# Performance work log

Measured on AMD Instinct MI355X. Metric: run time of the kernel, lower is better.

The kernel has to match this reference:

```python
import jax, jax.numpy as jnp
import numpy as np

B, T, C, H = 2, 2048, 1024, 16
HD = C // H  # head size = 64
EPS = 1e-5


def setup_inputs() -> dict:
    key = jax.random.key(0)
    ks = jax.random.split(key, 16)
    s = 0.02
    return {
        "x": jax.random.normal(ks[0], (B, T, C), jnp.float32),
        # per-head q/k/v projections, stacked: [H, C, HD]
        "Wq": jax.random.normal(ks[1], (H, C, HD), jnp.float32) * s,
        "Wk": jax.random.normal(ks[2], (H, C, HD), jnp.float32) * s,
        "Wv": jax.random.normal(ks[3], (H, C, HD), jnp.float32) * s,
        "Wproj": jax.random.normal(ks[4], (C, C), jnp.float32) * s,
        "bproj": jnp.zeros((C,), jnp.float32),
        "W1": jax.random.normal(ks[5], (C, 4 * C), jnp.float32) * s,
        "b1": jnp.zeros((4 * C,), jnp.float32),
        "W2": jax.random.normal(ks[6], (4 * C, C), jnp.float32) * s,
        "b2": jnp.zeros((C,), jnp.float32),
        "g1": jnp.ones((C,), jnp.float32),
        "be1": jnp.zeros((C,), jnp.float32),
        "g2": jnp.ones((C,), jnp.float32),
        "be2": jnp.zeros((C,), jnp.float32),
    }


def _layernorm(x, g, b):
    mu = jnp.mean(x, axis=-1, keepdims=True)
    var = jnp.mean(jnp.square(x - mu), axis=-1, keepdims=True)
    return (x - mu) * jax.lax.rsqrt(var + EPS) * g + b


def _block(x, Wq, Wk, Wv, Wproj, bproj, W1, b1, W2, b2, g1, be1, g2, be2):
    Bx, Tx, Cx = x.shape
    h = _layernorm(x, g1, be1)
    q = jnp.einsum("btc,hcd->bhtd", h, Wq)
    k = jnp.einsum("btc,hcd->bhtd", h, Wk)
    v = jnp.einsum("btc,hcd->bhtd", h, Wv)
    scores = jnp.einsum("bhtd,bhsd->bhts", q, k) * (HD ** -0.5)  # [B,H,T,T]
    causal = jnp.tril(jnp.ones((Tx, Tx), bool))
    scores = jnp.where(causal, scores, -jnp.inf)
    w = jax.nn.softmax(scores, axis=-1)
    o = jnp.einsum("bhts,bhsd->bhtd", w, v)
    o = o.transpose(0, 2, 1, 3).reshape(Bx, Tx, Cx)  # concat heads
    x = x + o @ Wproj + bproj
    h2 = _layernorm(x, g2, be2)
    ff = jax.nn.relu(h2 @ W1 + b1) @ W2 + b2
    return x + ff


def reference(x, Wq, Wk, Wv, Wproj, bproj, W1, b1, W2, b2, g1, be1, g2, be2):
    return _block(x, Wq, Wk, Wv, Wproj, bproj, W1, b1, W2, b2, g1, be1, g2, be2)
```

## Files before the change

### kernel.cpp

```cpp
#include <hip/hip_runtime.h>
#include <stdint.h>


typedef unsigned short u16;
typedef unsigned int u32;
typedef __attribute__((ext_vector_type(4))) float f32x4;
typedef __attribute__((ext_vector_type(8))) short s16x8;

__device__ __forceinline__ u16 f2bf(float f) {
  u32 u = __builtin_bit_cast(u32, f);
  u += 0x7fffu + ((u >> 16) & 1u);
  return (u16)(u >> 16);
}
__device__ __forceinline__ s16x8 ld_s16x8_a8(const u16* p) {
  union { uint2 d[2]; s16x8 v; } u;
  u.d[0] = *(const uint2*)p;
  u.d[1] = *(const uint2*)(p + 4);
  return u.v;
}
__device__ __forceinline__ void gload16(const u16* g, u16* lds_base) {
  __builtin_amdgcn_global_load_lds(
      (const __attribute__((address_space(1))) void*)g,
      (__attribute__((address_space(3))) void*)lds_base, 16, 0, 0);
}

__global__ __launch_bounds__(256) void transpose_all_kernel(
    const float* __restrict__ Wq, const float* __restrict__ Wk,
    const float* __restrict__ Wv, const float* __restrict__ Wproj,
    const float* __restrict__ W1, const float* __restrict__ W2,
    u16* __restrict__ WqkvT, u16* __restrict__ WprojT,
    u16* __restrict__ W1T, u16* __restrict__ W2T) {
  const int bid = blockIdx.x;
  const float* src; u16* dst; int Ccols, dstStride, r0, c0;
  if (bid < 768) {
    const int sub = bid >> 8, rem = bid & 255;
    const int z = rem >> 4, y = rem & 15;
    src = (sub == 0 ? Wq : sub == 1 ? Wk : Wv) + (size_t)z * 65536;
    dst = WqkvT + (size_t)sub * 1024 * 1024 + (size_t)z * 65536;
    Ccols = 64; dstStride = 1024; r0 = y * 64; c0 = 0;
  } else if (bid < 1024) {
    const int rem = bid - 768, xx = rem & 15, y = rem >> 4;
    src = Wproj; dst = WprojT; Ccols = 1024; dstStride = 1024;
    r0 = y * 64; c0 = xx * 64;
  } else if (bid < 2048) {
    const int rem = bid - 1024, xx = rem & 63, y = rem >> 6;
    src = W1; dst = W1T; Ccols = 4096; dstStride = 1024;
    r0 = y * 64; c0 = xx * 64;
  } else {
    const int rem = bid - 2048, xx = rem & 15, y = rem >> 4;
    src = W2; dst = W2T; Ccols = 1024; dstStride = 4096;
    r0 = y * 64; c0 = xx * 64;
  }
  __shared__ float t[64][65];
  const int tr = threadIdx.x >> 4, tc4 = (threadIdx.x & 15) * 4;
#pragma unroll
  for (int p = 0; p < 4; ++p) {
    int r = p * 16 + tr;
    float4 v = *(const float4*)(src + (size_t)(r0 + r) * Ccols + c0 + tc4);
    t[r][tc4 + 0] = v.x; t[r][tc4 + 1] = v.y;
    t[r][tc4 + 2] = v.z; t[r][tc4 + 3] = v.w;
  }
  __syncthreads();
#pragma unroll
  for (int p = 0; p < 4; ++p) {
    int c = p * 16 + tr;
    uint2 pk;
    pk.x = (u32)f2bf(t[tc4 + 0][c]) | ((u32)f2bf(t[tc4 + 1][c]) << 16);
    pk.y = (u32)f2bf(t[tc4 + 2][c]) | ((u32)f2bf(t[tc4 + 3][c]) << 16);
    *(uint2*)(dst + (size_t)(c0 + c) * dstStride + r0 + tc4) = pk;
  }
}

__global__ __launch_bounds__(256) void ln_kernel(
    const float* __restrict__ x, const float* __restrict__ g,
    const float* __restrict__ be, u16* __restrict__ out) {
  const int row = blockIdx.x, tid = threadIdx.x;
  const float* xr = x + (size_t)row * 1024;
  float4 v = *(const float4*)(xr + tid * 4);
  float s = v.x + v.y + v.z + v.w;
  float q = v.x * v.x + v.y * v.y + v.z * v.z + v.w * v.w;
#pragma unroll
  for (int off = 32; off > 0; off >>= 1) {
    s += __shfl_down(s, off);
    q += __shfl_down(q, off);
  }
  __shared__ float red[8];
  const int wid = tid >> 6, lane = tid & 63;
  if (lane == 0) { red[wid] = s; red[wid + 4] = q; }
  __syncthreads();
  s = red[0] + red[1] + red[2] + red[3];
  q = red[4] + red[5] + red[6] + red[7];
  const float mu = s * (1.f / 1024.f);
  const float var = q * (1.f / 1024.f) - mu * mu;
  const float rs = rsqrtf(var + 1e-5f);
  float4 gv = *(const float4*)(g + tid * 4);
  float4 bv = *(const float4*)(be + tid * 4);
  float o0 = (v.x - mu) * rs * gv.x + bv.x;
  float o1 = (v.y - mu) * rs * gv.y + bv.y;
  float o2 = (v.z - mu) * rs * gv.z + bv.z;
  float o3 = (v.w - mu) * rs * gv.w + bv.w;
  uint2 pk;
  pk.x = (u32)f2bf(o0) | ((u32)f2bf(o1) << 16);
  pk.y = (u32)f2bf(o2) | ((u32)f2bf(o3) << 16);
  *(uint2*)(out + (size_t)row * 1024 + tid * 4) = pk;
}

__global__ __launch_bounds__(256) void combine_kernel(
    const float* __restrict__ P, const float* __restrict__ resid,
    const float* __restrict__ bias, float* __restrict__ out) {
  const int row = blockIdx.x, c4 = threadIdx.x * 4;
  const size_t idx = (size_t)row * 1024 + c4;
  float4 p0 = *(const float4*)(P + idx);
  float4 p1 = *(const float4*)(P + 4194304 + idx);
  float4 r  = *(const float4*)(resid + idx);
  float4 bb = *(const float4*)(bias + c4);
  float4 o;
  o.x = p0.x + p1.x + r.x + bb.x;
  o.y = p0.y + p1.y + r.y + bb.y;
  o.z = p0.z + p1.z + r.z + bb.z;
  o.w = p0.w + p1.w + r.w + bb.w;
  *(float4*)(out + idx) = o;
}

template <int EPI>
__global__ __launch_bounds__(512, 2) void gemm256_kernel(
    const u16* __restrict__ A, const u16* __restrict__ BT,
    const float* __restrict__ bias, const float* __restrict__ resid,
    void* __restrict__ out, int M, int N, int K) {
  __shared__ u16 lds[2][2][256][64];
  const int tid = threadIdx.x;
  const int wid = tid >> 6, lane = tid & 63;
  const int m0 = blockIdx.y * 256, n0 = blockIdx.x * 256;
  const int wr = (wid >> 2) * 128;
  const int wc = (wid & 3) * 64;
  const int l15 = lane & 15, g = lane >> 4;
  const int lr = lane >> 3;
  const int cswz = ((lane & 7) * 8) ^ (lr << 3);
  const int swz = (l15 & 7) << 3;
  const u16* Abase = A + (size_t)m0 * K;
  const u16* Bbase = BT + (size_t)n0 * K;
  const int nkt = K >> 6;

  f32x4 acc[8][4] = {};
  s16x8 bf[4][2];

  auto issue_half = [&](const u16* Xbase, int xi, int t, int hf) {
    const int b = t & 1;
    const int r0 = hf * 128 + wid * 8;
    gload16(Xbase + (size_t)(r0 + lr) * K + t * 64 + cswz, &lds[b][xi][r0][0]);
    gload16(Xbase + (size_t)(r0 + 64 + lr) * K + t * 64 + cswz, &lds[b][xi][r0 + 64][0]);
  };

  issue_half(Abase, 0, 0, 0);
  issue_half(Abase, 0, 0, 1);
  issue_half(Bbase, 1, 0, 0);
  issue_half(Bbase, 1, 0, 1);
  asm volatile("s_waitcnt vmcnt(0)" ::: "memory");
  __builtin_amdgcn_s_barrier();

  for (int i = 0; i < nkt; i += 2) {
#pragma unroll
    for (int p = 0; p < 4; ++p) {
      s16x8 af[2][2];
#pragma unroll
      for (int q = 0; q < 2; ++q) {
        const int R = wr + (2 * p + q) * 16 + l15;
#pragma unroll
        for (int h = 0; h < 2; ++h)
          af[q][h] = *(const s16x8*)(&lds[0][0][R][(h * 32 + g * 8) ^ swz]);
      }
      if (p == 0) {
#pragma unroll
        for (int n = 0; n < 4; ++n) {
          const int R = wc + n * 16 + l15;
#pragma unroll
          for (int h = 0; h < 2; ++h)
            bf[n][h] = *(const s16x8*)(&lds[0][1][R][(h * 32 + g * 8) ^ swz]);
        }
      }
      if (i + 1 < nkt) {
        if (p == 0) issue_half(Abase, 0, i + 1, 0);
        else if (p == 1) issue_half(Abase, 0, i + 1, 1);
        else if (p == 2) issue_half(Bbase, 1, i + 1, 0);
        else issue_half(Bbase, 1, i + 1, 1);
      }
      __builtin_amdgcn_s_barrier();
      asm volatile("s_waitcnt lgkmcnt(0)" ::: "memory");
      __builtin_amdgcn_sched_barrier(0);
      __builtin_amdgcn_s_setprio(1);
#pragma unroll
      for (int q = 0; q < 2; ++q)
#pragma unroll
        for (int n = 0; n < 4; ++n) {
          acc[2 * p + q][n] = __builtin_amdgcn_mfma_f32_16x16x32_bf16(af[q][0], bf[n][0], acc[2 * p + q][n], 0, 0, 0);
          acc[2 * p + q][n] = __builtin_amdgcn_mfma_f32_16x16x32_bf16(af[q][1], bf[n][1], acc[2 * p + q][n], 0, 0, 0);
        }
      __builtin_amdgcn_s_setprio(0);
      if (p == 3)
        asm volatile("s_waitcnt vmcnt(0)" ::: "memory");
      __builtin_amdgcn_s_barrier();
    }
    if (i + 1 < nkt) {
#pragma unroll
      for (int p = 0; p < 4; ++p) {
        s16x8 af[2][2];
#pragma unroll
        for (int q = 0; q < 2; ++q) {
          const int R = wr + (2 * p + q) * 16 + l15;
#pragma unroll
          for (int h = 0; h < 2; ++h)
            af[q][h] = *(const s16x8*)(&lds[1][0][R][(h * 32 + g * 8) ^ swz]);
        }
        if (p == 0) {
#pragma unroll
          for (int n = 0; n < 4; ++n) {
            const int R = wc + n * 16 + l15;
#pragma unroll
            for (int h = 0; h < 2; ++h)
              bf[n][h] = *(const s16x8*)(&lds[1][1][R][(h * 32 + g * 8) ^ swz]);
          }
        }
        if (i + 2 < nkt) {
          if (p == 0) issue_half(Abase, 0, i + 2, 0);
          else if (p == 1) issue_half(Abase, 0, i + 2, 1);
          else if (p == 2) issue_half(Bbase, 1, i + 2, 0);
          else issue_half(Bbase, 1, i + 2, 1);
        }
        __builtin_amdgcn_s_barrier();
        asm volatile("s_waitcnt lgkmcnt(0)" ::: "memory");
        __builtin_amdgcn_sched_barrier(0);
        __builtin_amdgcn_s_setprio(1);
#pragma unroll
        for (int q = 0; q < 2; ++q)
#pragma unroll
          for (int n = 0; n < 4; ++n) {
            acc[2 * p + q][n] = __builtin_amdgcn_mfma_f32_16x16x32_bf16(af[q][0], bf[n][0], acc[2 * p + q][n], 0, 0, 0);
            acc[2 * p + q][n] = __builtin_amdgcn_mfma_f32_16x16x32_bf16(af[q][1], bf[n][1], acc[2 * p + q][n], 0, 0, 0);
          }
        __builtin_amdgcn_s_setprio(0);
        if (p == 3)
          asm volatile("s_waitcnt vmcnt(0)" ::: "memory");
        __builtin_amdgcn_s_barrier();
      }
    }
  }

#pragma unroll
  for (int mi = 0; mi < 8; ++mi)
#pragma unroll
    for (int n = 0; n < 4; ++n) {
      const int col = n0 + wc + n * 16 + l15;
      float bv = (EPI >= 1) ? bias[col] : 0.f;
#pragma unroll
      for (int ii = 0; ii < 4; ++ii) {
        const int row = m0 + wr + mi * 16 + g * 4 + ii;
        float v = acc[mi][n][ii];
        if (EPI >= 1) v += bv;
        if (EPI == 1) v = fmaxf(v, 0.f);
        ((u16*)out)[(size_t)row * N + col] = f2bf(v);
      }
    }
}

template <int EPI>
__global__ __launch_bounds__(256, 2) void gemm128d_kernel(
    const u16* __restrict__ A, const u16* __restrict__ BT,
    const float* __restrict__ bias, const float* __restrict__ resid,
    void* __restrict__ out, int M, int N, int K, int lda) {
  __shared__ u16 lds[2][2][128][64];
  const int tid = threadIdx.x;
  const int wid = tid >> 6, lane = tid & 63;
  const int m0 = blockIdx.y * 128, n0 = blockIdx.x * 128;
  const int wr = (wid >> 1) * 64, wc = (wid & 1) * 64;
  const int l15 = lane & 15, g = lane >> 4;
  const int lr = lane >> 3;
  const int cswz = ((lane & 7) * 8) ^ (lr << 3);
  const int swz = (l15 & 7) << 3;
  const int nkt = K >> 6;
  f32x4 acc[4][4] = {};

  if (EPI == 3) {
    const int koff = (int)blockIdx.z * K;
    A += koff; BT += koff;
  }

  auto stage = [&](int bsel, int t) {
#pragma unroll
    for (int p = 0; p < 4; ++p) {
      const int row = (p * 4 + wid) * 8;
      gload16(A + (size_t)(m0 + row + lr) * lda + t * 64 + cswz, &lds[bsel][0][row][0]);
    }
#pragma unroll
    for (int p = 0; p < 4; ++p) {
      const int row = (p * 4 + wid) * 8;
      gload16(BT + (size_t)(n0 + row + lr) * lda + t * 64 + cswz, &lds[bsel][1][row][0]);
    }
  };

  stage(0, 0);
  __syncthreads();

  int cur = 0;
  for (int i = 0; i < nkt; ++i) {
    if (i + 1 < nkt) stage(cur ^ 1, i + 1);
    s16x8 af[4][2], bf[4][2];
#pragma unroll
    for (int m = 0; m < 4; ++m) {
      const int R = wr + m * 16 + l15;
#pragma unroll
      for (int h = 0; h < 2; ++h)
        af[m][h] = *(const s16x8*)(&lds[cur][0][R][(h * 32 + g * 8) ^ swz]);
    }
#pragma unroll
    for (int n = 0; n < 4; ++n) {
      const int R = wc + n * 16 + l15;
#pragma unroll
      for (int h = 0; h < 2; ++h)
        bf[n][h] = *(const s16x8*)(&lds[cur][1][R][(h * 32 + g * 8) ^ swz]);
    }
    __builtin_amdgcn_s_setprio(1);
#pragma unroll
    for (int m = 0; m < 4; ++m)
#pragma unroll
      for (int n = 0; n < 4; ++n) {
        acc[m][n] = __builtin_amdgcn_mfma_f32_16x16x32_bf16(af[m][0], bf[n][0], acc[m][n], 0, 0, 0);
        acc[m][n] = __builtin_amdgcn_mfma_f32_16x16x32_bf16(af[m][1], bf[n][1], acc[m][n], 0, 0, 0);
      }
    __builtin_amdgcn_s_setprio(0);
    __syncthreads();
    cur ^= 1;
  }

  float* outf = (float*)out;
  if (EPI == 3) outf += (size_t)blockIdx.z * M * N;
#pragma unroll
  for (int m = 0; m < 4; ++m) {
#pragma unroll
    for (int n = 0; n < 4; ++n) {
      const int col = n0 + wc + n * 16 + l15;
      float bv = (EPI == 1 || EPI == 2) ? bias[col] : 0.f;
#pragma unroll
      for (int i = 0; i < 4; ++i) {
        const int row = m0 + wr + m * 16 + g * 4 + i;
        float v = acc[m][n][i];
        if (EPI == 1 || EPI == 2) v += bv;
        if (EPI == 1) v = fmaxf(v, 0.f);
        if (EPI == 2) {
          v += resid[(size_t)row * N + col];
          outf[(size_t)row * N + col] = v;
        } else if (EPI == 3) {
          outf[(size_t)row * N + col] = v;
        } else {
          ((u16*)out)[(size_t)row * N + col] = f2bf(v);
        }
      }
    }
  }
}

__global__ __launch_bounds__(512) void attn_mfma_kernel(
    const u16* __restrict__ qkv, u16* __restrict__ o) {
  __shared__ u16 sK[2][64][72];
  __shared__ u16 sVt[2][64][68];
  __shared__ u16 sP[8][16][72];
  const int tid = threadIdx.x;
  const int lid = (int)blockIdx.x;
  const int bh = lid & 31;
  const int qb = (lid < 256) ? (15 - ((lid >> 5) & 7)) : ((lid - 256) >> 5);
  const int b = bh >> 4, h = bh & 15;
  const int w = tid >> 6, lane = tid & 63;
  const int l15 = lane & 15, g = lane >> 4;
  const float c = 0.125f * 1.4426950408889634f;
  const int ks_r = tid >> 3, ks_c = (tid & 7) * 8;
  const int vs_s = tid & 63, vs_d = (tid >> 6) * 8;
  const u16* kbase = qkv + (size_t)(b * 2048) * 3072 + 1024 + h * 64;
  const u16* vbase = kbase + 1024;
  const int qw = qb * 128 + w * 16;

  const size_t qrow = (size_t)(b * 2048 + qw + l15);
  s16x8 qf0 = *(const s16x8*)(qkv + qrow * 3072 + h * 64 + g * 8);
  s16x8 qf1 = *(const s16x8*)(qkv + qrow * 3072 + h * 64 + 32 + g * 8);

  f32x4 oacc[4] = {};
  float mrow[4] = {-1e30f, -1e30f, -1e30f, -1e30f};
  float lrow[4] = {0.f, 0.f, 0.f, 0.f};

  const int nt = 2 * qb + 2;
  uint4 kr0, vr0;
  {
    const u16* kp = kbase + (size_t)(ks_r)*3072 + ks_c;
    kr0 = *(const uint4*)kp;
    const u16* vp = vbase + (size_t)(vs_s)*3072 + vs_d;
    vr0 = *(const uint4*)vp;
  }
  for (int t = 0; t < nt; ++t) {
    const int pb = t & 1;
    *(uint4*)(&sK[pb][ks_r][ks_c]) = kr0;
    {
      union { uint4 q4; u16 e[8]; } va;
      va.q4 = vr0;
#pragma unroll
      for (int j = 0; j < 8; ++j) sVt[pb][vs_d + j][vs_s] = va.e[j];
    }
    if (t + 1 < nt) {
      const u16* kp = kbase + (size_t)((t + 1) * 64 + ks_r) * 3072 + ks_c;
      kr0 = *(const uint4*)kp;
      const u16* vp = vbase + (size_t)((t + 1) * 64 + vs_s) * 3072 + vs_d;
      vr0 = *(const uint4*)vp;
    }
    __syncthreads();

    f32x4 st[4];
#pragma unroll
    for (int n = 0; n < 4; ++n) {
      s16x8 k0 = *(const s16x8*)(&sK[pb][n * 16 + l15][g * 8]);
      s16x8 k1 = *(const s16x8*)(&sK[pb][n * 16 + l15][32 + g * 8]);
      f32x4 a = {};
      a = __builtin_amdgcn_mfma_f32_16x16x32_bf16(qf0, k0, a, 0, 0, 0);
      a = __builtin_amdgcn_mfma_f32_16x16x32_bf16(qf1, k1, a, 0, 0, 0);
      st[n] = a;
    }
    if (t >= 2 * qb) {
#pragma unroll
      for (int n = 0; n < 4; ++n)
#pragma unroll
        for (int i = 0; i < 4; ++i) {
          const int s_abs = t * 64 + n * 16 + l15;
          const int q_abs = qw + 4 * g + i;
          if (s_abs > q_abs) st[n][i] = -1e30f;
        }
    }
    float pm[4];
#pragma unroll
    for (int i = 0; i < 4; ++i)
      pm[i] = fmaxf(fmaxf(st[0][i], st[1][i]), fmaxf(st[2][i], st[3][i]));
#pragma unroll
    for (int msk = 1; msk < 16; msk <<= 1)
#pragma unroll
      for (int i = 0; i < 4; ++i) pm[i] = fmaxf(pm[i], __shfl_xor(pm[i], msk));
    bool need = false;
#pragma unroll
    for (int i = 0; i < 4; ++i) need = need || (pm[i] > mrow[i] + 12.f);
    if (__any(need)) {
#pragma unroll
      for (int i = 0; i < 4; ++i) {
        const float mnew = fmaxf(mrow[i], pm[i]);
        const float corr = exp2f((mrow[i] - mnew) * c);
        mrow[i] = mnew;
        lrow[i] *= corr;
#pragma unroll
        for (int dt = 0; dt < 4; ++dt) oacc[dt][i] *= corr;
      }
    }
    float p[4][4];
#pragma unroll
    for (int n = 0; n < 4; ++n)
#pragma unroll
      for (int i = 0; i < 4; ++i) p[n][i] = exp2f((st[n][i] - mrow[i]) * c);
#pragma unroll
    for (int i = 0; i < 4; ++i)
      lrow[i] += (p[0][i] + p[1][i]) + (p[2][i] + p[3][i]);
#pragma unroll
    for (int n = 0; n < 4; ++n)
#pragma unroll
      for (int i = 0; i < 4; ++i)
        sP[w][4 * g + i][n * 16 + l15] = f2bf(p[n][i]);
    s16x8 pf0 = *(const s16x8*)(&sP[w][l15][g * 8]);
    s16x8 pf1 = *(const s16x8*)(&sP[w][l15][32 + g * 8]);
#pragma unroll
    for (int dt = 0; dt < 4; ++dt) {
      s16x8 vf0 = ld_s16x8_a8(&sVt[pb][dt * 16 + l15][g * 8]);
      s16x8 vf1 = ld_s16x8_a8(&sVt[pb][dt * 16 + l15][32 + g * 8]);
      oacc[dt] = __builtin_amdgcn_mfma_f32_16x16x32_bf16(pf0, vf0, oacc[dt], 0, 0, 0);
      oacc[dt] = __builtin_amdgcn_mfma_f32_16x16x32_bf16(pf1, vf1, oacc[dt], 0, 0, 0);
    }
  }

#pragma unroll
  for (int msk = 1; msk < 16; msk <<= 1)
#pragma unroll
    for (int i = 0; i < 4; ++i) lrow[i] += __shfl_xor(lrow[i], msk);
  float inv[4];
#pragma unroll
  for (int i = 0; i < 4; ++i) inv[i] = 1.f / lrow[i];
#pragma unroll
  for (int dt = 0; dt < 4; ++dt)
#pragma unroll
    for (int i = 0; i < 4; ++i) {
      const size_t row = (size_t)(b * 2048 + qw + 4 * g + i);
      o[row * 1024 + h * 64 + dt * 16 + l15] = f2bf(oacc[dt][i] * inv[i]);
    }
}

extern "C" void kernel_launch(void* const* d_in, const int* in_sizes, int n_in,
                              void* d_out, int out_size, void* d_ws, size_t ws_size,
                              hipStream_t stream) {
  const float* x     = (const float*)d_in[0];
  const float* Wq    = (const float*)d_in[1];
  const float* Wk    = (const float*)d_in[2];
  const float* Wv    = (const float*)d_in[3];
  const float* Wproj = (const float*)d_in[4];
  const float* bproj = (const float*)d_in[5];
  const float* W1    = (const float*)d_in[6];
  const float* b1    = (const float*)d_in[7];
  const float* W2    = (const float*)d_in[8];
  const float* b2    = (const float*)d_in[9];
  const float* g1    = (const float*)d_in[10];
  const float* be1   = (const float*)d_in[11];
  const float* g2    = (const float*)d_in[12];
  const float* be2   = (const float*)d_in[13];
  float* out = (float*)d_out;

  u16* WqkvT  = (u16*)d_ws;
  u16* WprojT = WqkvT + (size_t)3072 * 1024;
  u16* W1T    = WprojT + (size_t)1024 * 1024;
  u16* W2T    = W1T + (size_t)4096 * 1024;
  u16* hbuf   = W2T + (size_t)1024 * 4096;
  u16* qkv    = hbuf + (size_t)4096 * 1024;
  u16* obuf   = qkv + (size_t)4096 * 3072;
  float* x2   = (float*)(obuf + (size_t)4096 * 1024);
  u16* a1     = (u16*)(x2 + (size_t)4096 * 1024);
  float* Pk   = (float*)hbuf;

  transpose_all_kernel<<<3072, 256, 0, stream>>>(Wq, Wk, Wv, Wproj, W1, W2,
                                                 WqkvT, WprojT, W1T, W2T);
  ln_kernel<<<4096, 256, 0, stream>>>(x, g1, be1, hbuf);
  gemm256_kernel<0><<<dim3(12, 16), 512, 0, stream>>>(hbuf, WqkvT, nullptr, nullptr, qkv, 4096, 3072, 1024);
  attn_mfma_kernel<<<512, 512, 0, stream>>>(qkv, obuf);
  gemm128d_kernel<2><<<dim3(8, 32), 256, 0, stream>>>(obuf, WprojT, bproj, x, x2, 4096, 1024, 1024, 1024);
  ln_kernel<<<4096, 256, 0, stream>>>(x2, g2, be2, hbuf);
  gemm256_kernel<1><<<dim3(16, 16), 512, 0, stream>>>(hbuf, W1T, b1, nullptr, a1, 4096, 4096, 1024);
  gemm128d_kernel<3><<<dim3(8, 32, 2), 256, 0, stream>>>(a1, W2T, nullptr, nullptr, Pk, 4096, 1024, 2048, 4096);
  combine_kernel<<<4096, 256, 0, stream>>>(Pk, x2, b2, out);
}
```

Baseline: 236.2 us.

## Split long causal attention query blocks across two workgroups with merge kernel

Query blocks in the second half of the sequence now have their KV range split into two halves, each processed by its own workgroup. Each half writes unnormalized fp32 partial outputs plus row max and sum into scratch, and a new merge kernel combines them using log-sum-exp rescaling. The goal is to balance the causal triangle's uneven per-block work across 768 workgroups so the long blocks no longer set the tail. The cost is an extra kernel launch, the fp32 partial traffic, and reuse of the a1 workspace as scratch.

```diff
diff --git a/kernel.cpp b/kernel.cpp
--- a/kernel.cpp
+++ b/kernel.cpp
@@ -358,16 +358,25 @@
   }
 }
 
-__global__ __launch_bounds__(512) void attn_mfma_kernel(
-    const u16* __restrict__ qkv, u16* __restrict__ o) {
+__global__ __launch_bounds__(512) void attn_split_kernel(
+    const u16* __restrict__ qkv, u16* __restrict__ o,
+    float* __restrict__ Opart, float* __restrict__ mpart,
+    float* __restrict__ lpart) {
   __shared__ u16 sK[2][64][72];
   __shared__ u16 sVt[2][64][68];
   __shared__ u16 sP[8][16][72];
   const int tid = threadIdx.x;
   const int lid = (int)blockIdx.x;
-  const int bh = lid & 31;
-  const int qb = (lid < 256) ? (15 - ((lid >> 5) & 7)) : ((lid - 256) >> 5);
+  const int bh = lid & 31, slot = lid >> 5;
   const int b = bh >> 4, h = bh & 15;
+  int qb, t0, t1, half = 0; bool split;
+  if (slot < 8) { qb = slot; t0 = 0; t1 = 2 * qb + 2; split = false; }
+  else {
+    const int idx = slot - 8;
+    qb = 8 + (idx >> 1); half = idx & 1;
+    const int ntt = 2 * qb + 2, hlen = ntt >> 1;
+    t0 = half ? hlen : 0; t1 = half ? ntt : hlen; split = true;
+  }
   const int w = tid >> 6, lane = tid & 63;
   const int l15 = lane & 15, g = lane >> 4;
   const float c = 0.125f * 1.4426950408889634f;
@@ -385,15 +394,14 @@
   float mrow[4] = {-1e30f, -1e30f, -1e30f, -1e30f};
   float lrow[4] = {0.f, 0.f, 0.f, 0.f};
 
-  const int nt = 2 * qb + 2;
   uint4 kr0, vr0;
   {
-    const u16* kp = kbase + (size_t)(ks_r)*3072 + ks_c;
+    const u16* kp = kbase + (size_t)(t0 * 64 + ks_r) * 3072 + ks_c;
     kr0 = *(const uint4*)kp;
-    const u16* vp = vbase + (size_t)(vs_s)*3072 + vs_d;
+    const u16* vp = vbase + (size_t)(t0 * 64 + vs_s) * 3072 + vs_d;
     vr0 = *(const uint4*)vp;
   }
-  for (int t = 0; t < nt; ++t) {
+  for (int t = t0; t < t1; ++t) {
     const int pb = t & 1;
     *(uint4*)(&sK[pb][ks_r][ks_c]) = kr0;
     {
@@ -402,7 +410,7 @@
 #pragma unroll
       for (int j = 0; j < 8; ++j) sVt[pb][vs_d + j][vs_s] = va.e[j];
     }
-    if (t + 1 < nt) {
+    if (t + 1 < t1) {
       const u16* kp = kbase + (size_t)((t + 1) * 64 + ks_r) * 3072 + ks_c;
       kr0 = *(const uint4*)kp;
       const u16* vp = vbase + (size_t)((t + 1) * 64 + vs_s) * 3072 + vs_d;
@@ -480,16 +488,69 @@
   for (int msk = 1; msk < 16; msk <<= 1)
 #pragma unroll
     for (int i = 0; i < 4; ++i) lrow[i] += __shfl_xor(lrow[i], msk);
-  float inv[4];
-#pragma unroll
-  for (int i = 0; i < 4; ++i) inv[i] = 1.f / lrow[i];
-#pragma unroll
-  for (int dt = 0; dt < 4; ++dt)
-#pragma unroll
-    for (int i = 0; i < 4; ++i) {
-      const size_t row = (size_t)(b * 2048 + qw + 4 * g + i);
-      o[row * 1024 + h * 64 + dt * 16 + l15] = f2bf(oacc[dt][i] * inv[i]);
-    }
+
+  if (!split) {
+    float inv[4];
+#pragma unroll
+    for (int i = 0; i < 4; ++i) inv[i] = 1.f / lrow[i];
+#pragma unroll
+    for (int dt = 0; dt < 4; ++dt)
+#pragma unroll
+      for (int i = 0; i < 4; ++i) {
+        const size_t row = (size_t)(b * 2048 + qw + 4 * g + i);
+        o[row * 1024 + h * 64 + dt * 16 + l15] = f2bf(oacc[dt][i] * inv[i]);
+      }
+  } else {
+    const int pslot = (bh * 8 + (qb - 8)) * 2 + half;
+    float* Ob = Opart + ((size_t)pslot * 128) * 64;
+#pragma unroll
+    for (int dt = 0; dt < 4; ++dt)
+#pragma unroll
+      for (int i = 0; i < 4; ++i) {
+        const int lrw = w * 16 + 4 * g + i;
+        Ob[(size_t)lrw * 64 + dt * 16 + l15] = oacc[dt][i];
+      }
+    if (l15 == 0) {
+#pragma unroll
+      for (int i = 0; i < 4; ++i) {
+        const int lrw = w * 16 + 4 * g + i;
+        mpart[pslot * 128 + lrw] = mrow[i];
+        lpart[pslot * 128 + lrw] = lrow[i];
+      }
+    }
+  }
+}
+
+__global__ __launch_bounds__(256) void attn_merge_kernel(
+    const float* __restrict__ Opart, const float* __restrict__ mpart,
+    const float* __restrict__ lpart, u16* __restrict__ o) {
+  const int bid = blockIdx.x;
+  const int bh = bid >> 3, j = bid & 7;
+  const int b = bh >> 4, h = bh & 15;
+  const int qb = 8 + j;
+  const int tid = threadIdx.x;
+  const int r = tid >> 1, c0 = (tid & 1) * 32;
+  const float c = 0.125f * 1.4426950408889634f;
+  const int p0 = (bh * 8 + j) * 2, p1 = p0 + 1;
+  const float m0 = mpart[p0 * 128 + r], m1 = mpart[p1 * 128 + r];
+  const float l0 = lpart[p0 * 128 + r], l1 = lpart[p1 * 128 + r];
+  const float mM = fmaxf(m0, m1);
+  const float w0 = exp2f((m0 - mM) * c), w1 = exp2f((m1 - mM) * c);
+  const float inv = 1.f / (l0 * w0 + l1 * w1);
+  const float* O0 = Opart + ((size_t)p0 * 128 + r) * 64 + c0;
+  const float* O1 = Opart + ((size_t)p1 * 128 + r) * 64 + c0;
+  u16* op = o + (size_t)(b * 2048 + qb * 128 + r) * 1024 + h * 64 + c0;
+#pragma unroll
+  for (int k = 0; k < 32; k += 4) {
+    float4 a = *(const float4*)(O0 + k);
+    float4 bb = *(const float4*)(O1 + k);
+    uint2 pk;
+    pk.x = (u32)f2bf((a.x * w0 + bb.x * w1) * inv) |
+           ((u32)f2bf((a.y * w0 + bb.y * w1) * inv) << 16);
+    pk.y = (u32)f2bf((a.z * w0 + bb.z * w1) * inv) |
+           ((u32)f2bf((a.w * w0 + bb.w * w1) * inv) << 16);
+    *(uint2*)(op + k) = pk;
+  }
 }
 
 extern "C" void kernel_launch(void* const* d_in, const int* in_sizes, int n_in,
@@ -521,12 +582,16 @@
   float* x2   = (float*)(obuf + (size_t)4096 * 1024);
   u16* a1     = (u16*)(x2 + (size_t)4096 * 1024);
   float* Pk   = (float*)hbuf;
+  float* Opart = (float*)a1;
+  float* mpart = Opart + (size_t)512 * 128 * 64;
+  float* lpart = mpart + (size_t)512 * 128;
 
   transpose_all_kernel<<<3072, 256, 0, stream>>>(Wq, Wk, Wv, Wproj, W1, W2,
                                                  WqkvT, WprojT, W1T, W2T);
   ln_kernel<<<4096, 256, 0, stream>>>(x, g1, be1, hbuf);
   gemm256_kernel<0><<<dim3(12, 16), 512, 0, stream>>>(hbuf, WqkvT, nullptr, nullptr, qkv, 4096, 3072, 1024);
-  attn_mfma_kernel<<<512, 512, 0, stream>>>(qkv, obuf);
+  attn_split_kernel<<<768, 512, 0, stream>>>(qkv, obuf, Opart, mpart, lpart);
+  attn_merge_kernel<<<256, 256, 0, stream>>>(Opart, mpart, lpart, obuf);
   gemm128d_kernel<2><<<dim3(8, 32), 256, 0, stream>>>(obuf, WprojT, bproj, x, x2, 4096, 1024, 1024, 1024);
   ln_kernel<<<4096, 256, 0, stream>>>(x2, g2, be2, hbuf);
   gemm256_kernel<1><<<dim3(16, 16), 512, 0, stream>>>(hbuf, W1T, b1, nullptr, a1, 4096, 4096, 1024);
```

Result: slower. 250.2 us (+5.9%).
